# Kernel tuning notes

Measured on AMD Instinct MI355X. Metric: run time of the kernel, lower is better.

The kernel has to match this reference:

```python
import jax, jax.numpy as jnp
import numpy as np

TOKENS, D_IN, D_OUT = 8192, 4096, 11008


def setup_inputs() -> dict:
    key = jax.random.key(0)
    k1, k2, k3, k4 = jax.random.split(key, 4)
    x = jax.random.normal(k1, (TOKENS, D_IN), dtype=jnp.float32)
    # int8-range quantized weight (stored int32; values in [-127, 127] simulated via [0,127])
    weight_q = jax.random.randint(k2, (D_OUT, D_IN), -127, 128, dtype=jnp.int32)
    # per-output-row scale (abs-max / 127), small positive values
    max_val = jax.random.uniform(k3, (D_OUT,), dtype=jnp.float32, minval=1e-3, maxval=0.02)
    bias = jax.random.normal(k4, (D_OUT,), dtype=jnp.float32)
    return {"x": x, "weight_q": weight_q, "max_val": max_val, "bias": bias}


def reference(x, weight_q, max_val, bias):
    # dequantize: w[o, i] = weight_q[o, i] * max_val[o]   (per-row scale)
    w = weight_q.astype(x.dtype) * max_val[:, None]          # [D_OUT, D_IN]
    # linear: y = x @ w.T + bias
    return jnp.einsum('ti,oi->to', x, w) + bias               # [TOKENS, D_OUT]
```

## Files before the change

kernel.cpp:

```cpp
#include <hip/hip_runtime.h>


#define M_TOK 8192
#define K_DIM 4096
#define N_OUT 11008
#define BM 256
#define BN 256
#define BK 64
#define NT (K_DIM / BK)
#define NBM (M_TOK / BM)
#define NBN (N_OUT / BN)
#define NWG (NBM * NBN)
#define SLOT 32768

typedef __attribute__((ext_vector_type(4))) int   i32x4;
typedef __attribute__((ext_vector_type(4))) float f32x4;
typedef __attribute__((ext_vector_type(4))) short bf16x4;
typedef __attribute__((ext_vector_type(8))) short bf16x8;
typedef unsigned short u16;
typedef signed char i8;
typedef unsigned char u8;

__global__ __launch_bounds__(256) void prep_fused(
    const float* __restrict__ x, i8* __restrict__ xq, float* __restrict__ sx,
    const int* __restrict__ win, i8* __restrict__ wout, long n16) {
  __shared__ float wmx[4];
  const int tid = threadIdx.x;
  if (blockIdx.x < M_TOK) {
    const int t = blockIdx.x;
    const float* row = x + (long)t * K_DIM;
    f32x4 v[4];
    float mx = 0.0f;
#pragma unroll
    for (int j = 0; j < 4; ++j) {
      v[j] = ((const f32x4*)row)[tid * 4 + j];
#pragma unroll
      for (int e = 0; e < 4; ++e) mx = fmaxf(mx, fabsf(v[j][e]));
    }
#pragma unroll
    for (int off = 32; off >= 1; off >>= 1) mx = fmaxf(mx, __shfl_xor(mx, off));
    if ((tid & 63) == 0) wmx[tid >> 6] = mx;
    __syncthreads();
    mx = fmaxf(fmaxf(wmx[0], wmx[1]), fmaxf(wmx[2], wmx[3]));
    const float sxinv = (mx > 0.0f) ? 127.0f / mx : 0.0f;
    if (tid == 0) sx[t] = (mx > 0.0f) ? mx / 127.0f : 0.0f;
    i32x4 out;
#pragma unroll
    for (int j = 0; j < 4; ++j) {
      int q0 = __float2int_rn(v[j][0] * sxinv);
      int q1 = __float2int_rn(v[j][1] * sxinv);
      int q2 = __float2int_rn(v[j][2] * sxinv);
      int q3 = __float2int_rn(v[j][3] * sxinv);
      q0 = max(-127, min(127, q0)); q1 = max(-127, min(127, q1));
      q2 = max(-127, min(127, q2)); q3 = max(-127, min(127, q3));
      out[j] = (q0 & 255) | ((q1 & 255) << 8) | ((q2 & 255) << 16) | ((q3 & 255) << 24);
    }
    ((i32x4*)(xq + (long)t * K_DIM))[tid] = out;
  } else {
    long i = (long)(blockIdx.x - M_TOK) * blockDim.x + tid;
    const long stride = 2048L * blockDim.x;
    for (; i < n16; i += stride) {
      i32x4 o;
#pragma unroll
      for (int j = 0; j < 4; ++j) {
        i32x4 w = ((const i32x4*)win)[i * 4 + j];
        o[j] = (w[0] & 255) | ((w[1] & 255) << 8) | ((w[2] & 255) << 16) | ((w[3] & 255) << 24);
      }
      ((i32x4*)wout)[i] = o;
    }
  }
}

__device__ __forceinline__ void gl_lds16(const i8* g, u8* l) {
  __builtin_amdgcn_global_load_lds(
      (const __attribute__((address_space(1))) void*)g,
      (__attribute__((address_space(3))) void*)l,
      16, 0, 0);
}

#define STAGE(T) do { \
    u8* wp = lds + ((T) & 3) * SLOT; \
    const int ko_ = (T) * BK; \
    gl_lds16(pA + ko_, wp + dwa); \
    gl_lds16(pB + ko_, wp + 16384 + dwa); \
  } while (0)

#define TILE(T, AFC, AFN, RA, ST, CNTASM) do { \
    const char* pb_ = ldsc + ((T) & 3) * SLOT + bbase; \
    i32x4 bv[4]; \
    _Pragma("unroll") \
    for (int n = 0; n < 4; ++n) bv[n] = *(const i32x4*)(pb_ + n * 1024); \
    if (RA) { \
      const char* pa1_ = ldsc + (((T) + 1) & 3) * SLOT + abase; \
      _Pragma("unroll") \
      for (int m = 0; m < 4; ++m) AFN[m] = *(const i32x4*)(pa1_ + m * 1024); \
    } \
    if (ST) STAGE((T) + 3); \
    __builtin_amdgcn_s_setprio(1); \
    _Pragma("unroll") \
    for (int n = 0; n < 4; ++n) \
      _Pragma("unroll") \
      for (int m = 0; m < 4; ++m) \
        acc[m][n] = __builtin_amdgcn_mfma_i32_16x16x64_i8(AFC[m], bv[n], acc[m][n], 0, 0, 0); \
    __builtin_amdgcn_s_setprio(0); \
    asm volatile(CNTASM ::: "memory"); \
    __builtin_amdgcn_sched_barrier(0); \
    __builtin_amdgcn_s_barrier(); \
  } while (0)

__global__ __launch_bounds__(1024, 4) void gemm_i8(
    const i8* __restrict__ A, const i8* __restrict__ B,
    const float* __restrict__ sx, const float* __restrict__ scale,
    const float* __restrict__ bias, float* __restrict__ C) {
  __shared__ u8 lds[4 * SLOT];

  const int tid  = threadIdx.x;
  const int lane = tid & 63;
  const int wave = tid >> 6;
  const int wm = wave >> 2;
  const int wn = wave & 3;

  const int swz = (blockIdx.x & 7) * (NWG / 8) + (blockIdx.x >> 3);
  const int bm = swz / NBN;
  const int bn = swz % NBN;
  const long m0 = (long)bm * BM;
  const long n0 = (long)bn * BN;

  const int rs = tid >> 2;
  const int cs = ((tid & 3) * 16) ^ (((tid >> 3) & 3) << 4);
  const i8* pA = A + (m0 + rs) * (long)K_DIM + cs;
  const i8* pB = B + (n0 + rs) * (long)K_DIM + cs;
  const int dwa = wave * 1024;

  const int inner = ((lane >> 4) * 16) ^ ((((lane & 15) >> 1) & 3) << 4);
  const int abase = (wm * 64 + (lane & 15)) * 64 + inner;
  const int bbase = 16384 + (wn * 64 + (lane & 15)) * 64 + inner;
  const char* ldsc = (const char*)lds;

  i32x4 acc[4][4] = {};
  i32x4 afE[4], afO[4];

  STAGE(0); STAGE(1); STAGE(2);
  asm volatile("s_waitcnt vmcnt(2)" ::: "memory");
  __builtin_amdgcn_sched_barrier(0);
  __builtin_amdgcn_s_barrier();
  {
    const char* qa = ldsc + abase;
#pragma unroll
    for (int m = 0; m < 4; ++m) afE[m] = *(const i32x4*)(qa + m * 1024);
  }

  for (int t = 0; t < 60; t += 2) {
    TILE(t,     afE, afO, 1, 1, "s_waitcnt vmcnt(2)");
    TILE(t + 1, afO, afE, 1, 1, "s_waitcnt vmcnt(2)");
  }
  TILE(60, afE, afO, 1, 1, "s_waitcnt vmcnt(2)");
  TILE(61, afO, afE, 1, 0, "s_waitcnt vmcnt(0)");
  TILE(62, afE, afO, 1, 0, "s_waitcnt vmcnt(0)");
  TILE(63, afO, afE, 0, 0, "s_waitcnt vmcnt(0)");

  const int crow = (lane >> 4) * 4;
  const int ccol = lane & 15;
  float sxa[4][4];
#pragma unroll
  for (int m = 0; m < 4; ++m)
#pragma unroll
    for (int v = 0; v < 4; ++v)
      sxa[m][v] = sx[m0 + wm * 64 + m * 16 + crow + v];
#pragma unroll
  for (int n = 0; n < 4; ++n) {
    const long col = n0 + wn * 64 + n * 16 + ccol;
    const float sc = scale[col];
    const float bz = bias[col];
#pragma unroll
    for (int m = 0; m < 4; ++m) {
      const long row = m0 + wm * 64 + m * 16 + crow;
      i32x4 a = acc[m][n];
#pragma unroll
      for (int v = 0; v < 4; ++v)
        C[(row + v) * (long)N_OUT + col] = (float)a[v] * (sc * sxa[m][v]) + bz;
    }
  }
}

__device__ __forceinline__ u16 to_bf16_rne(float f) {
  union { float f; unsigned u; } v; v.f = f;
  return (u16)((v.u + 0x7FFFu + ((v.u >> 16) & 1u)) >> 16);
}

__global__ __launch_bounds__(256) void gemm_cvt(
    const float* __restrict__ X, const int* __restrict__ W,
    const float* __restrict__ scale, const float* __restrict__ bias,
    float* __restrict__ C) {
  __shared__ u16 lds_a[128 * 32];
  __shared__ u16 lds_b[128 * 32];

  const int tid  = threadIdx.x;
  const int lane = tid & 63;
  const int wave = tid >> 6;
  const int wm = wave >> 1, wn = wave & 1;

  const long m0 = (long)blockIdx.y * 128;
  const long n0 = (long)blockIdx.x * 128;

  const int arow = tid >> 3;
  const int acol = (tid & 7) * 4;

  const float* gX = X + (m0 + arow) * (long)K_DIM + acol;
  const int*   gW = W + (n0 + arow) * (long)K_DIM + acol;

  u16* wla = lds_a + arow * 32 + acol;
  u16* wlb = lds_b + arow * 32 + acol;

  f32x4 acc[4][4] = {};
  const int fr = lane & 15;
  const int fk = (lane >> 4) * 8;
  const u16* fa = lds_a + (wm * 64 + fr) * 32 + fk;
  const u16* fb = lds_b + (wn * 64 + fr) * 32 + fk;

  for (int kk = 0; kk < K_DIM / 32; ++kk) {
    const long ko = (long)kk * 32;
    f32x4 xv[4]; i32x4 wv[4];
#pragma unroll
    for (int j = 0; j < 4; ++j) {
      xv[j] = *(const f32x4*)(gX + (long)j * 32 * K_DIM + ko);
      wv[j] = *(const i32x4*)(gW + (long)j * 32 * K_DIM + ko);
    }
    __syncthreads();
#pragma unroll
    for (int j = 0; j < 4; ++j) {
      bf16x4 oa, ob;
      oa.x = (short)to_bf16_rne(xv[j][0]);
      oa.y = (short)to_bf16_rne(xv[j][1]);
      oa.z = (short)to_bf16_rne(xv[j][2]);
      oa.w = (short)to_bf16_rne(xv[j][3]);
      ob.x = (short)to_bf16_rne((float)wv[j][0]);
      ob.y = (short)to_bf16_rne((float)wv[j][1]);
      ob.z = (short)to_bf16_rne((float)wv[j][2]);
      ob.w = (short)to_bf16_rne((float)wv[j][3]);
      *(bf16x4*)(wla + j * 32 * 32) = oa;
      *(bf16x4*)(wlb + j * 32 * 32) = ob;
    }
    __syncthreads();

    bf16x8 af[4], bfr[4];
#pragma unroll
    for (int m = 0; m < 4; ++m) af[m] = *(const bf16x8*)(fa + m * 16 * 32);
#pragma unroll
    for (int n = 0; n < 4; ++n) bfr[n] = *(const bf16x8*)(fb + n * 16 * 32);
#pragma unroll
    for (int m = 0; m < 4; ++m)
#pragma unroll
      for (int n = 0; n < 4; ++n)
        acc[m][n] = __builtin_amdgcn_mfma_f32_16x16x32_bf16(af[m], bfr[n], acc[m][n], 0, 0, 0);
  }

  const int crow = (lane >> 4) * 4;
  const int ccol = lane & 15;
#pragma unroll
  for (int n = 0; n < 4; ++n) {
    const long col = n0 + wn * 64 + n * 16 + ccol;
    const float sc = scale[col];
    const float bz = bias[col];
#pragma unroll
    for (int m = 0; m < 4; ++m) {
      const long row = m0 + wm * 64 + m * 16 + crow;
      f32x4 a = acc[m][n];
#pragma unroll
      for (int v = 0; v < 4; ++v)
        C[(row + v) * (long)N_OUT + col] = a[v] * sc + bz;
    }
  }
}

extern "C" void kernel_launch(void* const* d_in, const int* in_sizes, int n_in,
                              void* d_out, int out_size, void* d_ws, size_t ws_size,
                              hipStream_t stream) {
  const float* x  = (const float*)d_in[0];
  const int*   wq = (const int*)d_in[1];
  const float* mx = (const float*)d_in[2];
  const float* bs = (const float*)d_in[3];
  float* out = (float*)d_out;

  const size_t szXQ = (size_t)M_TOK * K_DIM;
  const size_t szWQ = (size_t)N_OUT * K_DIM;
  const size_t szSX = (size_t)M_TOK * sizeof(float);
  if (ws_size >= szXQ + szWQ + szSX) {
    i8* xq = (i8*)d_ws;
    i8* wq8 = xq + szXQ;
    float* sx = (float*)(wq8 + szWQ);
    prep_fused<<<M_TOK + 2048, 256, 0, stream>>>(x, xq, sx, wq, wq8,
                                                 (long)N_OUT * K_DIM / 16);
    gemm_i8<<<dim3(NWG), dim3(1024), 0, stream>>>(xq, wq8, sx, mx, bs, out);
  } else {
    dim3 grid(N_OUT / 128, M_TOK / 128);
    gemm_cvt<<<grid, 256, 0, stream>>>(x, wq, mx, bs, out);
  }
}
```

Before: 511.3 us.

## Load A fragments directly from global into registers, stage only B in LDS

A-operand fragments are now read straight from global memory into registers one tile ahead, and only the B tile goes through the LDS ring buffer, which halves the LDS slot size. The waitcnt is moved before the MFMA block and its counts are adjusted for the extra outstanding vector loads, and the MFMA loop order is swapped to m-outer. The aim is to cut LDS footprint and LDS read traffic, possibly allowing more occupancy. The cost is uncoalesced 16-byte global loads per lane for A with no reuse across the four N-waves, plus an earlier wait that may expose memory latency. The loop already waits on loads issued one iteration earlier, but the vmcnt accounting is fragile.

New measurement: 1.172 ms. 2.29x slower.

```diff
diff --git a/kernel.cpp b/kernel.cpp
--- a/kernel.cpp
+++ b/kernel.cpp
@@ -11,7 +11,7 @@
 #define NBM (M_TOK / BM)
 #define NBN (N_OUT / BN)
 #define NWG (NBM * NBN)
-#define SLOT 32768
+#define SLOT 16384
 
 typedef __attribute__((ext_vector_type(4))) int   i32x4;
 typedef __attribute__((ext_vector_type(4))) float f32x4;
@@ -79,10 +79,7 @@
 }
 
 #define STAGE(T) do { \
-    u8* wp = lds + ((T) & 3) * SLOT; \
-    const int ko_ = (T) * BK; \
-    gl_lds16(pA + ko_, wp + dwa); \
-    gl_lds16(pB + ko_, wp + 16384 + dwa); \
+    gl_lds16(pB + (T) * BK, lds + ((T) & 3) * SLOT + dwa); \
   } while (0)
 
 #define TILE(T, AFC, AFN, RA, ST, CNTASM) do { \
@@ -91,19 +88,20 @@
     _Pragma("unroll") \
     for (int n = 0; n < 4; ++n) bv[n] = *(const i32x4*)(pb_ + n * 1024); \
     if (RA) { \
-      const char* pa1_ = ldsc + (((T) + 1) & 3) * SLOT + abase; \
+      const long ko1_ = (long)((T) + 1) * BK; \
       _Pragma("unroll") \
-      for (int m = 0; m < 4; ++m) AFN[m] = *(const i32x4*)(pa1_ + m * 1024); \
+      for (int m = 0; m < 4; ++m) AFN[m] = *(const i32x4*)(pAf[m] + ko1_); \
     } \
     if (ST) STAGE((T) + 3); \
+    asm volatile(CNTASM ::: "memory"); \
+    __builtin_amdgcn_sched_barrier(0); \
     __builtin_amdgcn_s_setprio(1); \
     _Pragma("unroll") \
-    for (int n = 0; n < 4; ++n) \
+    for (int m = 0; m < 4; ++m) \
       _Pragma("unroll") \
-      for (int m = 0; m < 4; ++m) \
+      for (int n = 0; n < 4; ++n) \
         acc[m][n] = __builtin_amdgcn_mfma_i32_16x16x64_i8(AFC[m], bv[n], acc[m][n], 0, 0, 0); \
     __builtin_amdgcn_s_setprio(0); \
-    asm volatile(CNTASM ::: "memory"); \
     __builtin_amdgcn_sched_barrier(0); \
     __builtin_amdgcn_s_barrier(); \
   } while (0)
@@ -128,36 +126,36 @@
 
   const int rs = tid >> 2;
   const int cs = ((tid & 3) * 16) ^ (((tid >> 3) & 3) << 4);
-  const i8* pA = A + (m0 + rs) * (long)K_DIM + cs;
   const i8* pB = B + (n0 + rs) * (long)K_DIM + cs;
-  const int dwa = wave * 1024;
+  const int dwa = wave * 1024 + ((tid & 63) >> 6);
+
+  const i8* pAf[4];
+#pragma unroll
+  for (int m = 0; m < 4; ++m)
+    pAf[m] = A + (m0 + wm * 64 + m * 16 + (lane & 15)) * (long)K_DIM + (lane >> 4) * 16;
 
   const int inner = ((lane >> 4) * 16) ^ ((((lane & 15) >> 1) & 3) << 4);
-  const int abase = (wm * 64 + (lane & 15)) * 64 + inner;
-  const int bbase = 16384 + (wn * 64 + (lane & 15)) * 64 + inner;
+  const int bbase = (wn * 64 + (lane & 15)) * 64 + inner;
   const char* ldsc = (const char*)lds;
 
   i32x4 acc[4][4] = {};
   i32x4 afE[4], afO[4];
 
+#pragma unroll
+  for (int m = 0; m < 4; ++m) afE[m] = *(const i32x4*)(pAf[m] + 0);
   STAGE(0); STAGE(1); STAGE(2);
   asm volatile("s_waitcnt vmcnt(2)" ::: "memory");
   __builtin_amdgcn_sched_barrier(0);
   __builtin_amdgcn_s_barrier();
-  {
-    const char* qa = ldsc + abase;
-#pragma unroll
-    for (int m = 0; m < 4; ++m) afE[m] = *(const i32x4*)(qa + m * 1024);
-  }
 
   for (int t = 0; t < 60; t += 2) {
-    TILE(t,     afE, afO, 1, 1, "s_waitcnt vmcnt(2)");
-    TILE(t + 1, afO, afE, 1, 1, "s_waitcnt vmcnt(2)");
-  }
-  TILE(60, afE, afO, 1, 1, "s_waitcnt vmcnt(2)");
-  TILE(61, afO, afE, 1, 0, "s_waitcnt vmcnt(0)");
-  TILE(62, afE, afO, 1, 0, "s_waitcnt vmcnt(0)");
-  TILE(63, afO, afE, 0, 0, "s_waitcnt vmcnt(0)");
+    TILE(t,     afE, afO, 1, 1, "s_waitcnt vmcnt(6) lgkmcnt(0)");
+    TILE(t + 1, afO, afE, 1, 1, "s_waitcnt vmcnt(6) lgkmcnt(0)");
+  }
+  TILE(60, afE, afO, 1, 1, "s_waitcnt vmcnt(6) lgkmcnt(0)");
+  TILE(61, afO, afE, 1, 0, "s_waitcnt vmcnt(5) lgkmcnt(0)");
+  TILE(62, afE, afO, 1, 0, "s_waitcnt vmcnt(4) lgkmcnt(0)");
+  TILE(63, afO, afE, 0, 0, "s_waitcnt vmcnt(0) lgkmcnt(0)");
 
   const int crow = (lane >> 4) * 4;
   const int ccol = lane & 15;
```
